# Performance work log

Hardware: AMD Instinct MI355X
Metric: run time of the kernel (lower is better)

The kernel has to match this reference:

```python
import jax, jax.numpy as jnp
import numpy as np

BIG = 1e10  # sentinel for invalid pairwise distances


def get_xyz(depth, fx, fy, cx, cy):
    # depth: [B,1,H,W] -> xyz: [B,3,H,W] via pinhole unprojection
    B, _, H, W = depth.shape
    v = jnp.arange(H, dtype=depth.dtype)[:, None]   # rows
    u = jnp.arange(W, dtype=depth.dtype)[None, :]   # cols
    z = depth[:, 0]                                  # [B,H,W]
    x = (u - cx) / fx * z
    y = (v - cy) / fy * z
    return jnp.stack([x, y, z], axis=1)              # [B,3,H,W]


def _chamfer_item(p, g, vp, vg):
    # p,g: [N,3] point sets; vp,vg: [N] bool validity masks
    # squared pairwise distances via ||p||^2 + ||g||^2 - 2 p.g
    d = (jnp.sum(p * p, -1)[:, None] + jnp.sum(g * g, -1)[None, :]
         - 2.0 * (p @ g.T))                          # [N,N]
    d = jnp.maximum(d, 0.0)
    has_g = jnp.any(vg)
    has_p = jnp.any(vp)
    d1 = jnp.min(jnp.where(vg[None, :], d, BIG), axis=1)  # per pred point
    d2 = jnp.min(jnp.where(vp[:, None], d, BIG), axis=0)  # per gt point
    s1 = jnp.sum(jnp.where(vp & has_g, d1, 0.0))
    s2 = jnp.sum(jnp.where(vg & has_p, d2, 0.0))
    return s1 + s2


def reference(pred, gt_xyz, mask, fx, fy, cx, cy):
    B = pred.shape[0]
    pred_xyz = get_xyz(pred, fx, fy, cx, cy)             # [B,3,H,W]
    p = pred_xyz.reshape(B, 3, -1).transpose(0, 2, 1)    # [B,N,3]
    g = gt_xyz.reshape(B, 3, -1).transpose(0, 2, 1)      # [B,N,3]
    m = mask[:, 0].reshape(B, -1) > 0                    # [B,N]
    # ignore_zeros=True: drop points whose coordinate sum is exactly 0
    vp = m & (jnp.sum(p, -1) != 0)
    vg = m & (jnp.sum(g, -1) != 0)
    per_item = jax.vmap(_chamfer_item)(p, g, vp, vg)     # [B]
    return jnp.sum(per_item) / B


def setup_inputs() -> dict:
    key = jax.random.key(0)
    k1, k2, k3 = jax.random.split(key, 3)
    B, H, W = 2, 128, 128
    pred = jax.random.uniform(k1, (B, 1, H, W), dtype=jnp.float32) * 2.0 + 0.1
    gt_xyz = jax.random.normal(k2, (B, 3, H, W), dtype=jnp.float32)
    mask = jax.random.randint(k3, (B, 1, H, W), 0, 2, dtype=jnp.int32)
    fx = jnp.float32(525.0)
    fy = jnp.float32(525.0)
    cx = jnp.float32(64.0)
    cy = jnp.float32(64.0)
    return {"pred": pred, "gt_xyz": gt_xyz, "mask": mask,
            "fx": fx, "fy": fy, "cx": cx, "cy": cy}
```

## Files before the change

kernel.cpp:

```cpp
#include <hip/hip_runtime.h>

#define B_ITEMS 2
#define W_IMG   128
#define N_PTS   16384
#define CH_GRID 1024

__global__ __launch_bounds__(256) void prep_kernel(
        const float* __restrict__ pred,
        const float* __restrict__ gt,
        const int*   __restrict__ mask,
        const float* fxp, const float* fyp,
        const float* cxp, const float* cyp,
        int*    __restrict__ cnt,
        float4* __restrict__ pR, float4* __restrict__ gR,
        float4* __restrict__ pT, float4* __restrict__ gT,
        float*  __restrict__ out) {
    int s    = blockIdx.x >> 6;
    int b    = s & 1;
    int isG  = s >> 1;
    int tid  = threadIdx.x;
    int idx  = (blockIdx.x & 63) * 256 + tid;
    int lane = tid & 63, w = tid >> 6;

    if (blockIdx.x == 0 && tid == 0) out[0] = 0.0f;

    float x, y, z;
    if (!isG) {
        float fx = *fxp, fy = *fyp, cx = *cxp, cy = *cyp;
        float u = (float)(idx & (W_IMG - 1));
        float v = (float)(idx >> 7);
        z = pred[b * N_PTS + idx];
        x = (u - cx) / fx * z;
        y = (v - cy) / fy * z;
    } else {
        x = gt[(b * 3 + 0) * N_PTS + idx];
        y = gt[(b * 3 + 1) * N_PTS + idx];
        z = gt[(b * 3 + 2) * N_PTS + idx];
    }
    int  mv = mask[b * N_PTS + idx];
    bool ok = (mv > 0) && (((x + y) + z) != 0.0f);

    unsigned long long bal = __ballot(ok);
    int nw  = __popcll(bal);
    int pre = __popcll(bal & ((1ull << lane) - 1ull));

    __shared__ int wbase[4];
    __shared__ int blockbase;
    if (lane == 0) wbase[w] = nw;
    __syncthreads();
    if (tid == 0) {
        int s0 = 0;
#pragma unroll
        for (int i = 0; i < 4; ++i) { int t = wbase[i]; wbase[i] = s0; s0 += t; }
        blockbase = s0 ? atomicAdd(&cnt[s], s0) : 0;
    }
    __syncthreads();

    if (ok) {
        int pos = blockbase + wbase[w] + pre;
        float ps = fmaf(z, z, fmaf(y, y, x * x));
        float4* __restrict__ raw = (isG ? gR : pR) + b * N_PTS;
        float4* __restrict__ tf  = (isG ? gT : pT) + b * N_PTS;
        raw[pos] = make_float4(x, y, z, ps);
        tf[pos]  = make_float4(-2.0f * x, -2.0f * y, -2.0f * z, ps);
    }
}

__global__ __launch_bounds__(256, 4) void chamfer_kernel(
        const int*    __restrict__ cnt,
        const float4* __restrict__ pR, const float4* __restrict__ gR,
        const float4* __restrict__ pT, const float4* __restrict__ gT,
        float* __restrict__ out) {
    int np0 = cnt[0], np1 = cnt[1], ng0 = cnt[2], ng1 = cnt[3];
    int naArr[4] = {np0, ng0, np1, ng1};
    int nbArr[4] = {ng0, np0, ng1, np1};
    const float4* Arow[4] = {pR, gR, pR + N_PTS, gR + N_PTS};
    const float4* Bcol[4] = {gT, pT, gT + N_PTS, pT + N_PTS};

    int units[4];
    int Utot = 0;
#pragma unroll
    for (int i = 0; i < 4; ++i) {
        units[i] = (naArr[i] > 0 && nbArr[i] > 0) ? ((naArr[i] + 63) >> 6) : 0;
        Utot += units[i];
    }
    int u = blockIdx.x;
    if (u >= Utot) return;
    int s = 0;
    while (u >= units[s]) { u -= units[s]; ++s; }
    int na = naArr[s], nb = nbArr[s];
    const float4* __restrict__ A  = Arow[s];
    const float4* __restrict__ Bp = Bcol[s];
    int rowbase = u * 64;

    int tid = threadIdx.x;
    int tc = tid & 31, tr = tid >> 5;

    float px[8], py[8], pz[8], rm[8];
#pragma unroll
    for (int a = 0; a < 8; ++a) {
        float4 v = A[rowbase + a * 8 + tr];
        px[a] = v.x; py[a] = v.y; pz[a] = v.z;
        rm[a] = 3.4e38f;
    }

    __shared__ float4 sB[2][512];
    __shared__ float  smin[64];
    int ntiles = (nb + 511) >> 9;

#pragma unroll
    for (int k = 0; k < 2; ++k) {
        int j = k * 256 + tid;
        float4 v = Bp[min(j, N_PTS - 1)];
        bool okc = j < nb;
        float4 r;
        r.x = okc ? v.x : 0.0f;
        r.y = okc ? v.y : 0.0f;
        r.z = okc ? v.z : 0.0f;
        r.w = okc ? v.w : 3.4e38f;
        sB[0][k * 256 + tid] = r;
    }
    __syncthreads();

    for (int t = 0; t < ntiles; ++t) {
        float4 r0, r1;
        bool have = (t + 1 < ntiles);
        if (have) {
            int j0 = (t + 1) * 512 + tid;
            int j1 = j0 + 256;
            float4 v0 = Bp[min(j0, N_PTS - 1)];
            float4 v1 = Bp[min(j1, N_PTS - 1)];
            bool k0 = j0 < nb, k1 = j1 < nb;
            r0.x = k0 ? v0.x : 0.0f; r0.y = k0 ? v0.y : 0.0f;
            r0.z = k0 ? v0.z : 0.0f; r0.w = k0 ? v0.w : 3.4e38f;
            r1.x = k1 ? v1.x : 0.0f; r1.y = k1 ? v1.y : 0.0f;
            r1.z = k1 ? v1.z : 0.0f; r1.w = k1 ? v1.w : 3.4e38f;
        }
        const float4* __restrict__ buf = sB[t & 1] + tc;
#pragma unroll
        for (int cb = 0; cb < 16; ++cb) {
            float4 c = buf[cb * 32];
#pragma unroll
            for (int a = 0; a < 8; ++a)
                rm[a] = fminf(rm[a],
                    fmaf(px[a], c.x, fmaf(py[a], c.y, fmaf(pz[a], c.z, c.w))));
        }
        if (have) {
            sB[(t + 1) & 1][tid] = r0;
            sB[(t + 1) & 1][256 + tid] = r1;
        }
        __syncthreads();
    }

#pragma unroll
    for (int a = 0; a < 8; ++a) {
        float v = rm[a];
        v = fminf(v, __shfl_xor(v, 1, 64));
        v = fminf(v, __shfl_xor(v, 2, 64));
        v = fminf(v, __shfl_xor(v, 4, 64));
        v = fminf(v, __shfl_xor(v, 8, 64));
        v = fminf(v, __shfl_xor(v, 16, 64));
        rm[a] = v;
    }
    if (tc == 0) {
#pragma unroll
        for (int a = 0; a < 8; ++a) smin[a * 8 + tr] = rm[a];
    }
    __syncthreads();
    if (tid < 64) {
        int row = rowbase + tid;
        float v  = smin[tid];
        float ps = A[row].w;
        float contrib = (row < na) ? fmaxf(v + ps, 0.0f) : 0.0f;
#pragma unroll
        for (int off = 32; off > 0; off >>= 1)
            contrib += __shfl_down(contrib, off, 64);
        if (tid == 0) atomicAdd(out, contrib * (1.0f / B_ITEMS));
    }
}

extern "C" void kernel_launch(void* const* d_in, const int* in_sizes, int n_in,
                              void* d_out, int out_size, void* d_ws, size_t ws_size,
                              hipStream_t stream) {
    const float* pred = (const float*)d_in[0];
    const float* gt   = (const float*)d_in[1];
    const int*   mask = (const int*)  d_in[2];
    const float* fx   = (const float*)d_in[3];
    const float* fy   = (const float*)d_in[4];
    const float* cx   = (const float*)d_in[5];
    const float* cy   = (const float*)d_in[6];
    float* out = (float*)d_out;

    char* ws = (char*)d_ws;
    size_t SEG = (size_t)B_ITEMS * N_PTS * 16;
    int*    cnt = (int*)ws;
    float4* pR  = (float4*)(ws + 256);
    float4* gR  = (float4*)(ws + 256 + SEG);
    float4* pT  = (float4*)(ws + 256 + 2 * SEG);
    float4* gT  = (float4*)(ws + 256 + 3 * SEG);

    hipMemsetAsync(cnt, 0, 16, stream);

    prep_kernel<<<dim3(256), 256, 0, stream>>>(
        pred, gt, mask, fx, fy, cx, cy, cnt, pR, gR, pT, gT, out);

    chamfer_kernel<<<dim3(CH_GRID), 256, 0, stream>>>(
        cnt, pR, gR, pT, gT, out);
}
```

Baseline: 103.3 us.

## Split column range across two blocks per row tile with atomicMin merge

Each 64-row tile is now handled by two blocks, each scanning half of the opposing point set. Partial minima are merged with integer atomicMin into a global buffer, which the prep kernel initialises, and a new finish kernel reduces that buffer into the output. The change doubles the grid so more CUs stay busy, since there are only about 512 row tiles. It also drops bounds masking on full tiles and processes two columns per inner step. In exchange it adds a third kernel launch, global atomics, and reloads the row data in both blocks.

```diff
diff --git a/kernel.cpp b/kernel.cpp
--- a/kernel.cpp
+++ b/kernel.cpp
@@ -3,7 +3,8 @@
 #define B_ITEMS 2
 #define W_IMG   128
 #define N_PTS   16384
-#define CH_GRID 1024
+#define CH_GRID 2048
+#define BIGF    3.4e38f
 
 __global__ __launch_bounds__(256) void prep_kernel(
         const float* __restrict__ pred,
@@ -14,6 +15,7 @@
         int*    __restrict__ cnt,
         float4* __restrict__ pR, float4* __restrict__ gR,
         float4* __restrict__ pT, float4* __restrict__ gT,
+        float*  __restrict__ rmG,
         float*  __restrict__ out) {
     int s    = blockIdx.x >> 6;
     int b    = s & 1;
@@ -23,6 +25,7 @@
     int lane = tid & 63, w = tid >> 6;
 
     if (blockIdx.x == 0 && tid == 0) out[0] = 0.0f;
+    rmG[(blockIdx.x << 8) + tid] = BIGF;
 
     float x, y, z;
     if (!isG) {
@@ -70,7 +73,7 @@
         const int*    __restrict__ cnt,
         const float4* __restrict__ pR, const float4* __restrict__ gR,
         const float4* __restrict__ pT, const float4* __restrict__ gT,
-        float* __restrict__ out) {
+        float* __restrict__ rmG) {
     int np0 = cnt[0], np1 = cnt[1], ng0 = cnt[2], ng1 = cnt[3];
     int naArr[4] = {np0, ng0, np1, ng1};
     int nbArr[4] = {ng0, np0, ng1, np1};
@@ -81,7 +84,7 @@
     int Utot = 0;
 #pragma unroll
     for (int i = 0; i < 4; ++i) {
-        units[i] = (naArr[i] > 0 && nbArr[i] > 0) ? ((naArr[i] + 63) >> 6) : 0;
+        units[i] = (naArr[i] > 0 && nbArr[i] > 0) ? (2 * ((naArr[i] + 63) >> 6)) : 0;
         Utot += units[i];
     }
     int u = blockIdx.x;
@@ -91,7 +94,11 @@
     int na = naArr[s], nb = nbArr[s];
     const float4* __restrict__ A  = Arow[s];
     const float4* __restrict__ Bp = Bcol[s];
-    int rowbase = u * 64;
+    int h       = u & 1;
+    int rowbase = (u >> 1) * 64;
+    int half    = (nb + 1) >> 1;
+    int cbase   = h * half;
+    int ccount  = min(nb - cbase, half);
 
     int tid = threadIdx.x;
     int tc = tid & 31, tr = tid >> 5;
@@ -101,24 +108,29 @@
     for (int a = 0; a < 8; ++a) {
         float4 v = A[rowbase + a * 8 + tr];
         px[a] = v.x; py[a] = v.y; pz[a] = v.z;
-        rm[a] = 3.4e38f;
+        rm[a] = BIGF;
     }
 
     __shared__ float4 sB[2][512];
-    __shared__ float  smin[64];
-    int ntiles = (nb + 511) >> 9;
-
-#pragma unroll
-    for (int k = 0; k < 2; ++k) {
-        int j = k * 256 + tid;
-        float4 v = Bp[min(j, N_PTS - 1)];
-        bool okc = j < nb;
-        float4 r;
-        r.x = okc ? v.x : 0.0f;
-        r.y = okc ? v.y : 0.0f;
-        r.z = okc ? v.z : 0.0f;
-        r.w = okc ? v.w : 3.4e38f;
-        sB[0][k * 256 + tid] = r;
+    int ntiles = (ccount + 511) >> 9;
+
+    if (512 <= ccount) {
+#pragma unroll
+        for (int k = 0; k < 2; ++k)
+            sB[0][k * 256 + tid] = Bp[cbase + k * 256 + tid];
+    } else {
+#pragma unroll
+        for (int k = 0; k < 2; ++k) {
+            int j = k * 256 + tid;
+            float4 v = Bp[min(cbase + j, N_PTS - 1)];
+            bool okc = j < ccount;
+            float4 r;
+            r.x = okc ? v.x : 0.0f;
+            r.y = okc ? v.y : 0.0f;
+            r.z = okc ? v.z : 0.0f;
+            r.w = okc ? v.w : BIGF;
+            sB[0][k * 256 + tid] = r;
+        }
     }
     __syncthreads();
 
@@ -128,22 +140,32 @@
         if (have) {
             int j0 = (t + 1) * 512 + tid;
             int j1 = j0 + 256;
-            float4 v0 = Bp[min(j0, N_PTS - 1)];
-            float4 v1 = Bp[min(j1, N_PTS - 1)];
-            bool k0 = j0 < nb, k1 = j1 < nb;
-            r0.x = k0 ? v0.x : 0.0f; r0.y = k0 ? v0.y : 0.0f;
-            r0.z = k0 ? v0.z : 0.0f; r0.w = k0 ? v0.w : 3.4e38f;
-            r1.x = k1 ? v1.x : 0.0f; r1.y = k1 ? v1.y : 0.0f;
-            r1.z = k1 ? v1.z : 0.0f; r1.w = k1 ? v1.w : 3.4e38f;
-        }
-        const float4* __restrict__ buf = sB[t & 1] + tc;
-#pragma unroll
-        for (int cb = 0; cb < 16; ++cb) {
-            float4 c = buf[cb * 32];
-#pragma unroll
-            for (int a = 0; a < 8; ++a)
-                rm[a] = fminf(rm[a],
-                    fmaf(px[a], c.x, fmaf(py[a], c.y, fmaf(pz[a], c.z, c.w))));
+            if ((t + 2) * 512 <= ccount) {
+                r0 = Bp[cbase + j0];
+                r1 = Bp[cbase + j1];
+            } else {
+                float4 v0 = Bp[min(cbase + j0, N_PTS - 1)];
+                float4 v1 = Bp[min(cbase + j1, N_PTS - 1)];
+                bool k0 = j0 < ccount, k1 = j1 < ccount;
+                r0.x = k0 ? v0.x : 0.0f; r0.y = k0 ? v0.y : 0.0f;
+                r0.z = k0 ? v0.z : 0.0f; r0.w = k0 ? v0.w : BIGF;
+                r1.x = k1 ? v1.x : 0.0f; r1.y = k1 ? v1.y : 0.0f;
+                r1.z = k1 ? v1.z : 0.0f; r1.w = k1 ? v1.w : BIGF;
+            }
+        }
+        const float4* __restrict__ bufc = sB[t & 1] + tc;
+#pragma unroll
+        for (int cb = 0; cb < 8; ++cb) {
+            float4 c0 = bufc[cb * 64];
+            float4 c1 = bufc[cb * 64 + 32];
+#pragma unroll
+            for (int a = 0; a < 8; ++a) {
+                float d0 = fmaf(px[a], c0.x,
+                              fmaf(py[a], c0.y, fmaf(pz[a], c0.z, c0.w)));
+                float d1 = fmaf(px[a], c1.x,
+                              fmaf(py[a], c1.y, fmaf(pz[a], c1.z, c1.w)));
+                rm[a] = fminf(fminf(rm[a], d0), d1);
+            }
         }
         if (have) {
             sB[(t + 1) & 1][tid] = r0;
@@ -163,19 +185,39 @@
         rm[a] = v;
     }
     if (tc == 0) {
-#pragma unroll
-        for (int a = 0; a < 8; ++a) smin[a * 8 + tr] = rm[a];
-    }
-    __syncthreads();
-    if (tid < 64) {
-        int row = rowbase + tid;
-        float v  = smin[tid];
-        float ps = A[row].w;
-        float contrib = (row < na) ? fmaxf(v + ps, 0.0f) : 0.0f;
-#pragma unroll
-        for (int off = 32; off > 0; off >>= 1)
-            contrib += __shfl_down(contrib, off, 64);
-        if (tid == 0) atomicAdd(out, contrib * (1.0f / B_ITEMS));
+        int base = s << 14;
+#pragma unroll
+        for (int a = 0; a < 8; ++a) {
+            int row = rowbase + a * 8 + tr;
+            if (row < na) {
+                float ps = A[row].w;
+                float vr = fmaxf(rm[a] + ps, 0.0f);
+                atomicMin((int*)&rmG[base + row], __float_as_int(vr));
+            }
+        }
+    }
+}
+
+__global__ __launch_bounds__(256) void finish_kernel(
+        const int*   __restrict__ cnt,
+        const float* __restrict__ rmG,
+        float*       __restrict__ out) {
+    int gid = blockIdx.x * 256 + threadIdx.x;
+    int s   = gid >> 14;
+    int row = gid & (N_PTS - 1);
+    int np0 = cnt[0], np1 = cnt[1], ng0 = cnt[2], ng1 = cnt[3];
+    int naArr[4] = {np0, ng0, np1, ng1};
+    int nbArr[4] = {ng0, np0, ng1, np1};
+    float v = (row < naArr[s] && nbArr[s] > 0) ? rmG[gid] : 0.0f;
+#pragma unroll
+    for (int off = 32; off > 0; off >>= 1)
+        v += __shfl_down(v, off, 64);
+    __shared__ float wsum[4];
+    if ((threadIdx.x & 63) == 0) wsum[threadIdx.x >> 6] = v;
+    __syncthreads();
+    if (threadIdx.x == 0) {
+        float t = (wsum[0] + wsum[1]) + (wsum[2] + wsum[3]);
+        atomicAdd(out, t * (1.0f / B_ITEMS));
     }
 }
 
@@ -198,12 +240,15 @@
     float4* gR  = (float4*)(ws + 256 + SEG);
     float4* pT  = (float4*)(ws + 256 + 2 * SEG);
     float4* gT  = (float4*)(ws + 256 + 3 * SEG);
+    float*  rmG = (float*) (ws + 256 + 4 * SEG);
 
     hipMemsetAsync(cnt, 0, 16, stream);
 
     prep_kernel<<<dim3(256), 256, 0, stream>>>(
-        pred, gt, mask, fx, fy, cx, cy, cnt, pR, gR, pT, gT, out);
+        pred, gt, mask, fx, fy, cx, cy, cnt, pR, gR, pT, gT, rmG, out);
 
     chamfer_kernel<<<dim3(CH_GRID), 256, 0, stream>>>(
-        cnt, pR, gR, pT, gT, out);
-}
+        cnt, pR, gR, pT, gT, rmG);
+
+    finish_kernel<<<dim3(256), 256, 0, stream>>>(cnt, rmG, out);
+}
```

Result: no change. 104.1 us (+0.7%).

## Split chamfer columns across blocks and waves with atomicMin and last-block reduction

Applied to the files above, without the earlier changes.

The chamfer kernel now splits each 64-row unit's column range into four block-level quarters and then across the four waves in each block. This quadruples the grid and drops the shared-memory tiling, so each wave streams its columns directly from global memory with uniform (broadcast) loads. Per-row minima are combined with an integer atomicMin into a global buffer that the prep kernel initialises. A last-block-done counter then performs the final sum, replacing the per-block float atomicAdd. The aim is more parallelism and occupancy, at the cost of global atomics and scalar global loads instead of LDS reuse.

```diff
diff --git a/kernel.cpp b/kernel.cpp
--- a/kernel.cpp
+++ b/kernel.cpp
@@ -3,7 +3,9 @@
 #define B_ITEMS 2
 #define W_IMG   128
 #define N_PTS   16384
-#define CH_GRID 1024
+#define QS      4
+#define CH_GRID 4096
+#define BIGF    3.4e38f
 
 __global__ __launch_bounds__(256) void prep_kernel(
         const float* __restrict__ pred,
@@ -14,6 +16,7 @@
         int*    __restrict__ cnt,
         float4* __restrict__ pR, float4* __restrict__ gR,
         float4* __restrict__ pT, float4* __restrict__ gT,
+        float*  __restrict__ rmG,
         float*  __restrict__ out) {
     int s    = blockIdx.x >> 6;
     int b    = s & 1;
@@ -23,6 +26,7 @@
     int lane = tid & 63, w = tid >> 6;
 
     if (blockIdx.x == 0 && tid == 0) out[0] = 0.0f;
+    rmG[(blockIdx.x << 8) + tid] = BIGF;
 
     float x, y, z;
     if (!isG) {
@@ -66,10 +70,12 @@
     }
 }
 
-__global__ __launch_bounds__(256, 4) void chamfer_kernel(
+__global__ __launch_bounds__(256, 8) void chamfer_kernel(
         const int*    __restrict__ cnt,
         const float4* __restrict__ pR, const float4* __restrict__ gR,
         const float4* __restrict__ pT, const float4* __restrict__ gT,
+        float* __restrict__ rmG,
+        int*   __restrict__ done,
         float* __restrict__ out) {
     int np0 = cnt[0], np1 = cnt[1], ng0 = cnt[2], ng1 = cnt[3];
     int naArr[4] = {np0, ng0, np1, ng1};
@@ -81,101 +87,106 @@
     int Utot = 0;
 #pragma unroll
     for (int i = 0; i < 4; ++i) {
-        units[i] = (naArr[i] > 0 && nbArr[i] > 0) ? ((naArr[i] + 63) >> 6) : 0;
+        units[i] = (naArr[i] > 0 && nbArr[i] > 0) ? (((naArr[i] + 63) >> 6) * QS) : 0;
         Utot += units[i];
     }
+
+    int tid  = threadIdx.x;
+    int lane = tid & 63;
+    int w    = __builtin_amdgcn_readfirstlane(tid >> 6);
+
+    __shared__ float sm[4][64];
+    __shared__ float wsum[4];
+    __shared__ int   lastFlag;
+
     int u = blockIdx.x;
-    if (u >= Utot) return;
-    int s = 0;
-    while (u >= units[s]) { u -= units[s]; ++s; }
-    int na = naArr[s], nb = nbArr[s];
-    const float4* __restrict__ A  = Arow[s];
-    const float4* __restrict__ Bp = Bcol[s];
-    int rowbase = u * 64;
-
-    int tid = threadIdx.x;
-    int tc = tid & 31, tr = tid >> 5;
-
-    float px[8], py[8], pz[8], rm[8];
-#pragma unroll
-    for (int a = 0; a < 8; ++a) {
-        float4 v = A[rowbase + a * 8 + tr];
-        px[a] = v.x; py[a] = v.y; pz[a] = v.z;
-        rm[a] = 3.4e38f;
-    }
-
-    __shared__ float4 sB[2][512];
-    __shared__ float  smin[64];
-    int ntiles = (nb + 511) >> 9;
-
-#pragma unroll
-    for (int k = 0; k < 2; ++k) {
-        int j = k * 256 + tid;
-        float4 v = Bp[min(j, N_PTS - 1)];
-        bool okc = j < nb;
-        float4 r;
-        r.x = okc ? v.x : 0.0f;
-        r.y = okc ? v.y : 0.0f;
-        r.z = okc ? v.z : 0.0f;
-        r.w = okc ? v.w : 3.4e38f;
-        sB[0][k * 256 + tid] = r;
-    }
-    __syncthreads();
-
-    for (int t = 0; t < ntiles; ++t) {
-        float4 r0, r1;
-        bool have = (t + 1 < ntiles);
-        if (have) {
-            int j0 = (t + 1) * 512 + tid;
-            int j1 = j0 + 256;
-            float4 v0 = Bp[min(j0, N_PTS - 1)];
-            float4 v1 = Bp[min(j1, N_PTS - 1)];
-            bool k0 = j0 < nb, k1 = j1 < nb;
-            r0.x = k0 ? v0.x : 0.0f; r0.y = k0 ? v0.y : 0.0f;
-            r0.z = k0 ? v0.z : 0.0f; r0.w = k0 ? v0.w : 3.4e38f;
-            r1.x = k1 ? v1.x : 0.0f; r1.y = k1 ? v1.y : 0.0f;
-            r1.z = k1 ? v1.z : 0.0f; r1.w = k1 ? v1.w : 3.4e38f;
-        }
-        const float4* __restrict__ buf = sB[t & 1] + tc;
-#pragma unroll
-        for (int cb = 0; cb < 16; ++cb) {
-            float4 c = buf[cb * 32];
-#pragma unroll
-            for (int a = 0; a < 8; ++a)
-                rm[a] = fminf(rm[a],
-                    fmaf(px[a], c.x, fmaf(py[a], c.y, fmaf(pz[a], c.z, c.w))));
-        }
-        if (have) {
-            sB[(t + 1) & 1][tid] = r0;
-            sB[(t + 1) & 1][256 + tid] = r1;
-        }
+    if (u < Utot) {
+        int s = 0;
+        while (u >= units[s]) { u -= units[s]; ++s; }
+        int na = naArr[s], nb = nbArr[s];
+        const float4* __restrict__ A  = Arow[s];
+        const float4* __restrict__ Bp = Bcol[s];
+        int q       = u & (QS - 1);
+        int rowbase = (u >> 2) * 64;
+
+        int Lq  = (nb + QS - 1) >> 2;
+        int cb0 = q * Lq;
+        int cc  = min(nb - cb0, Lq); if (cc < 0) cc = 0;
+        int Lw  = (cc + 3) >> 2;
+        int wb  = cb0 + w * Lw;
+        int wc  = min(cc - w * Lw, Lw); if (wc < 0) wc = 0;
+
+        int    row = rowbase + lane;
+        float4 av  = A[row];
+        float  px = av.x, py = av.y, pz = av.z, ps = av.w;
+        float  rm = BIGF;
+
+        const float4* __restrict__ Bq = Bp + wb;
+
+#define CHPAIR(CA, CB) { \
+        float d0_ = fmaf(px, CA.x, fmaf(py, CA.y, fmaf(pz, CA.z, CA.w))); \
+        float d1_ = fmaf(px, CB.x, fmaf(py, CB.y, fmaf(pz, CB.z, CB.w))); \
+        rm = fminf(fminf(rm, d0_), d1_); }
+
+        int j = 0;
+#pragma unroll 1
+        for (; j + 8 <= wc; j += 8) {
+            float4 c0 = Bq[j + 0], c1 = Bq[j + 1];
+            float4 c2 = Bq[j + 2], c3 = Bq[j + 3];
+            float4 c4 = Bq[j + 4], c5 = Bq[j + 5];
+            float4 c6 = Bq[j + 6], c7 = Bq[j + 7];
+            CHPAIR(c0, c1)
+            CHPAIR(c2, c3)
+            CHPAIR(c4, c5)
+            CHPAIR(c6, c7)
+        }
+        for (; j < wc; ++j) {
+            float4 c = Bq[j];
+            float d = fmaf(px, c.x, fmaf(py, c.y, fmaf(pz, c.z, c.w)));
+            rm = fminf(rm, d);
+        }
+#undef CHPAIR
+
+        sm[w][lane] = rm;
         __syncthreads();
-    }
-
-#pragma unroll
-    for (int a = 0; a < 8; ++a) {
-        float v = rm[a];
-        v = fminf(v, __shfl_xor(v, 1, 64));
-        v = fminf(v, __shfl_xor(v, 2, 64));
-        v = fminf(v, __shfl_xor(v, 4, 64));
-        v = fminf(v, __shfl_xor(v, 8, 64));
-        v = fminf(v, __shfl_xor(v, 16, 64));
-        rm[a] = v;
-    }
-    if (tc == 0) {
-#pragma unroll
-        for (int a = 0; a < 8; ++a) smin[a * 8 + tr] = rm[a];
-    }
-    __syncthreads();
-    if (tid < 64) {
-        int row = rowbase + tid;
-        float v  = smin[tid];
-        float ps = A[row].w;
-        float contrib = (row < na) ? fmaxf(v + ps, 0.0f) : 0.0f;
+        if (tid < 64) {
+            float m = fminf(fminf(sm[0][tid], sm[1][tid]),
+                            fminf(sm[2][tid], sm[3][tid]));
+            int r2 = rowbase + tid;
+            if (r2 < na) {
+                float vr = fmaxf(m + ps, 0.0f);
+                atomicMin((int*)&rmG[(s << 14) + r2], __float_as_int(vr));
+            }
+        }
+    }
+
+    __syncthreads();
+    __threadfence();
+    if (tid == 0) {
+        int old = atomicAdd(done, 1);
+        lastFlag = (old == (int)gridDim.x - 1) ? 1 : 0;
+    }
+    __syncthreads();
+
+    if (lastFlag) {
+        int* rmGi = (int*)rmG;
+        float acc = 0.0f;
+#pragma unroll 1
+        for (int s2 = 0; s2 < 4; ++s2) {
+            if (nbArr[s2] <= 0) continue;
+            int na2  = naArr[s2];
+            int base = s2 << 14;
+            for (int k = tid; k < na2; k += 256)
+                acc += __int_as_float(__hip_atomic_load(&rmGi[base + k],
+                        __ATOMIC_RELAXED, __HIP_MEMORY_SCOPE_AGENT));
+        }
 #pragma unroll
         for (int off = 32; off > 0; off >>= 1)
-            contrib += __shfl_down(contrib, off, 64);
-        if (tid == 0) atomicAdd(out, contrib * (1.0f / B_ITEMS));
+            acc += __shfl_down(acc, off, 64);
+        if (lane == 0) wsum[w] = acc;
+        __syncthreads();
+        if (tid == 0)
+            out[0] = (wsum[0] + wsum[1] + wsum[2] + wsum[3]) * (1.0f / B_ITEMS);
     }
 }
 
@@ -193,17 +204,19 @@
 
     char* ws = (char*)d_ws;
     size_t SEG = (size_t)B_ITEMS * N_PTS * 16;
-    int*    cnt = (int*)ws;
-    float4* pR  = (float4*)(ws + 256);
-    float4* gR  = (float4*)(ws + 256 + SEG);
-    float4* pT  = (float4*)(ws + 256 + 2 * SEG);
-    float4* gT  = (float4*)(ws + 256 + 3 * SEG);
-
-    hipMemsetAsync(cnt, 0, 16, stream);
+    int*    cnt  = (int*)ws;
+    int*    done = cnt + 4;
+    float4* pR   = (float4*)(ws + 256);
+    float4* gR   = (float4*)(ws + 256 + SEG);
+    float4* pT   = (float4*)(ws + 256 + 2 * SEG);
+    float4* gT   = (float4*)(ws + 256 + 3 * SEG);
+    float*  rmG  = (float*) (ws + 256 + 4 * SEG);
+
+    hipMemsetAsync(cnt, 0, 32, stream);
 
     prep_kernel<<<dim3(256), 256, 0, stream>>>(
-        pred, gt, mask, fx, fy, cx, cy, cnt, pR, gR, pT, gT, out);
+        pred, gt, mask, fx, fy, cx, cy, cnt, pR, gR, pT, gT, rmG, out);
 
     chamfer_kernel<<<dim3(CH_GRID), 256, 0, stream>>>(
-        cnt, pR, gR, pT, gT, out);
+        cnt, pR, gR, pT, gT, rmG, done, out);
 }
```

After: 412.7 us. 3.99x slower.
